# Performance work log

Measured on AMD Instinct MI355X. Metric: run time of the kernel, lower is better.

Reference implementation:

```python
import jax, jax.numpy as jnp
import numpy as np

N_NODES = 100000


def _gcn_conv(x, W, b, src, dst, n):
    # PyG GCNConv: h = x @ W; add self-loops; norm = d^-1/2[src] * d^-1/2[dst];
    # out[i] = sum_{(s->i)} norm * h[s] + b
    h = x @ W  # [N, F_out]
    deg = jax.ops.segment_sum(jnp.ones_like(dst, dtype=h.dtype), dst, num_segments=n)
    dis = jnp.where(deg > 0, jax.lax.rsqrt(jnp.maximum(deg, 1.0)), 0.0)
    norm = dis[src] * dis[dst]  # [E]
    msg = h[src] * norm[:, None]  # [E, F_out] gather + scale
    out = jax.ops.segment_sum(msg, dst, num_segments=n)  # scatter-add
    return out + b


def _add_self_loops(edge_index, n):
    loops = jnp.arange(n, dtype=edge_index.dtype)
    src = jnp.concatenate([edge_index[0], loops])
    dst = jnp.concatenate([edge_index[1], loops])
    return src, dst


def setup_inputs() -> dict:
    key = jax.random.key(0)
    k_x, k_e, k_w1, k_w2 = jax.random.split(key, 4)
    n, e, f_in, f_hid = N_NODES, 1600000, 128, 64
    x = jax.random.normal(k_x, (n, f_in), dtype=jnp.float32)
    edge_index = jax.random.randint(k_e, (2, e), 0, n, dtype=jnp.int64)
    # Glorot-ish init for weights
    W1 = jax.random.normal(k_w1, (f_in, f_hid), dtype=jnp.float32) / np.sqrt(f_in)
    b1 = jnp.zeros((f_hid,), dtype=jnp.float32)
    W2 = jax.random.normal(k_w2, (f_hid, f_hid), dtype=jnp.float32) / np.sqrt(f_hid)
    b2 = jnp.zeros((f_hid,), dtype=jnp.float32)
    return {"x": x, "edge_index": edge_index, "W1": W1, "b1": b1, "W2": W2, "b2": b2}


def reference(x, edge_index, W1, b1, W2, b2):
    n = x.shape[0]
    src, dst = _add_self_loops(edge_index, n)
    h = jax.nn.relu(_gcn_conv(x, W1, b1, src, dst, n))
    # F.dropout(training=False) in eval mode is identity
    out = _gcn_conv(h, W2, b2, src, dst, n)
    return out
```

## Files before the change

### kernel.cpp

```cpp
#include <hip/hip_runtime.h>
#include <hip/hip_bf16.h>


#define FOUT 64
#define BW 128
#define BSH 7
#define MAXB 1024
#define NCHS 512
#define CHUNK 4096
#define SLAB 3072

#define NT1 1024
#define NT2 512
#define LCOLN 2048

__device__ __forceinline__ float bf2f(unsigned int u16) {
    union { unsigned int i; float f; } c;
    c.i = u16 << 16;
    return c.f;
}
__device__ __forceinline__ unsigned short f2bf(float f) {
    union { float f; unsigned int i; } c;
    c.f = f;
    unsigned int i = c.i;
    return (unsigned short)((i + 0x7FFFu + ((i >> 16) & 1u)) >> 16);
}

typedef __attribute__((ext_vector_type(8))) short short8v;
typedef __attribute__((ext_vector_type(4))) float f32x4;

__device__ __forceinline__ void split_frag(const float* xa, short8v* Ah, short8v* Al) {
    union { unsigned int u[4]; short8v v; } H, L;
#pragma unroll
    for (int p = 0; p < 4; p++) {
        unsigned short h0 = f2bf(xa[2 * p]);
        unsigned short h1 = f2bf(xa[2 * p + 1]);
        H.u[p] = (unsigned int)h0 | ((unsigned int)h1 << 16);
        unsigned short l0 = f2bf(xa[2 * p] - bf2f(h0));
        unsigned short l1 = f2bf(xa[2 * p + 1] - bf2f(h1));
        L.u[p] = (unsigned int)l0 | ((unsigned int)l1 << 16);
    }
    *Ah = H.v;
    *Al = L.v;
}

__device__ __forceinline__ void conv_w_frag(const float* __restrict__ W,
                                            unsigned short* __restrict__ WhF,
                                            unsigned short* __restrict__ WlF,
                                            int task) {
    const int lane = task & 63;
    const int cf = (task >> 6) & 3;
    const int s = task >> 8;
    const int q = lane >> 4, m = lane & 15;
#pragma unroll
    for (int j = 0; j < 8; j++) {
        int k = s * 32 + q * 8 + j;
        float x = W[(size_t)k * 64 + cf * 16 + m];
        unsigned short h = f2bf(x);
        WhF[(size_t)task * 8 + j] = h;
        WlF[(size_t)task * 8 + j] = f2bf(x - bf2f(h));
    }
}

__global__ __launch_bounds__(512) void edge_sort(
    const int* __restrict__ src, const int* __restrict__ dst, int E,
    int* __restrict__ pk, int* __restrict__ ebuf2,
    const float* __restrict__ W1, const float* __restrict__ W2,
    unsigned short* __restrict__ whf1, unsigned short* __restrict__ wlf1,
    unsigned short* __restrict__ whf2, unsigned short* __restrict__ wlf2) {
    __shared__ int h[MAXB];
    __shared__ int lbuf[CHUNK];
    __shared__ int wt8[8];
    const int blk = blockIdx.x, t = threadIdx.x;
    const int lane = t & 63, wv = t >> 6;
    const int e0 = blk * CHUNK;
    const int chunkE = min(CHUNK, E - e0);

    int ed[CHUNK / 512], es[CHUNK / 512];
#pragma unroll
    for (int k = 0; k < CHUNK / 512; k++) {
        int e = e0 + k * 512 + t;
        bool ok = (e < E);
        ed[k] = ok ? dst[e] : -1;
        es[k] = ok ? src[e] : 0;
    }
    h[t] = 0;
    h[t + 512] = 0;
    __syncthreads();
#pragma unroll
    for (int k = 0; k < CHUNK / 512; k++)
        if (ed[k] >= 0) atomicAdd(&h[ed[k] >> BSH], 1);
    if (blk == 0) {
        for (int task = t; task < NT1 + NT2; task += 512) {
            if (task < NT1) conv_w_frag(W1, whf1, wlf1, task);
            else            conv_w_frag(W2, whf2, wlf2, task - NT1);
        }
    }
    __syncthreads();
    const int c0 = h[t], c1 = h[t + 512];

    int pv = c0;
#pragma unroll
    for (int d = 1; d < 64; d <<= 1) {
        int x = __shfl_up(pv, d);
        if (lane >= d) pv += x;
    }
    if (lane == 63) wt8[wv] = pv;
    __syncthreads();
    int woff = 0, tot0 = 0;
#pragma unroll
    for (int ww = 0; ww < 8; ww++) {
        int vw = wt8[ww];
        if (ww < wv) woff += vw;
        tot0 += vw;
    }
    const int excl0 = woff + pv - c0;
    __syncthreads();
    int pv1 = c1;
#pragma unroll
    for (int d = 1; d < 64; d <<= 1) {
        int x = __shfl_up(pv1, d);
        if (lane >= d) pv1 += x;
    }
    if (lane == 63) wt8[wv] = pv1;
    __syncthreads();
    int woff1 = 0;
#pragma unroll
    for (int ww = 0; ww < 8; ww++)
        if (ww < wv) woff1 += wt8[ww];
    const int excl1 = tot0 + woff1 + pv1 - c1;

    pk[t * NCHS + blk] = (excl0 << 16) | c0;
    pk[(t + 512) * NCHS + blk] = (excl1 << 16) | c1;

    h[t] = excl0;
    h[t + 512] = excl1;
    __syncthreads();
#pragma unroll
    for (int k = 0; k < CHUNK / 512; k++)
        if (ed[k] >= 0) {
            int b = ed[k] >> BSH;
            int r = atomicAdd(&h[b], 1);
            lbuf[r] = es[k] | ((ed[k] & (BW - 1)) << 17);
        }
    __syncthreads();
#pragma unroll
    for (int k = 0; k < CHUNK / 512; k++) {
        int i = t + k * 512;
        if (i < chunkE) ebuf2[(size_t)blk * CHUNK + i] = lbuf[i];
    }
}

__global__ __launch_bounds__(256, 3) void csr_gemm(
    const int* __restrict__ pk, const int* __restrict__ ebuf2, int nch,
    int* __restrict__ ebuf, unsigned int* __restrict__ rowinfo,
    float* __restrict__ dis, int n,
    const float* __restrict__ X, const unsigned short* __restrict__ WhF,
    const unsigned short* __restrict__ WlF, unsigned short* __restrict__ HS) {
    __shared__ int ldeg[BW];
    __shared__ float sdis[BW];
    __shared__ int wt4[4];
    __shared__ int prefL[NCHS];
    __shared__ int loffL[NCHS];
    const int b = blockIdx.x, t = threadIdx.x;
    const int node0 = b << BSH;
    const int nn = min(BW, n - node0);
    const int ebeg = b * SLAB;

    const int lane = t & 63;
    const int wvv = t >> 6;
    const int m = lane & 15;
    const int q = lane >> 4;
    const int tile0 = wvv * 2, tile1 = wvv * 2 + 1;
    const int r0 = node0 + tile0 * 16 + m;
    const int r1 = node0 + tile1 * 16 + m;
    const bool ok0 = (r0 < n), ok1 = (r1 < n);
    const float* xp0 = X + (size_t)r0 * 128 + q * 8;
    const float* xp1 = X + (size_t)r1 * 128 + q * 8;
    const float4 zf4 = make_float4(0.f, 0.f, 0.f, 0.f);

    const int pkA = (t < nch) ? pk[b * NCHS + t] : 0;
    const int pkB = (t + 256 < nch) ? pk[b * NCHS + t + 256] : 0;
#define XDECL(S) float4 xa##S##_0, xa##S##_1, xb##S##_0, xb##S##_1;
    XDECL(0) XDECL(1) XDECL(2) XDECL(3)
#undef XDECL
#define XLOAD(S)                                                             \
    if (ok0) {                                                               \
        xa##S##_0 = *(const float4*)(xp0 + (S) * 32);                        \
        xa##S##_1 = *(const float4*)(xp0 + (S) * 32 + 4);                    \
    } else { xa##S##_0 = zf4; xa##S##_1 = zf4; }                             \
    if (ok1) {                                                               \
        xb##S##_0 = *(const float4*)(xp1 + (S) * 32);                        \
        xb##S##_1 = *(const float4*)(xp1 + (S) * 32 + 4);                    \
    } else { xb##S##_0 = zf4; xb##S##_1 = zf4; }
    XLOAD(0) XLOAD(1) XLOAD(2) XLOAD(3)
#undef XLOAD

    const int cA = pkA & 0xFFFF, cB = pkB & 0xFFFF;
    int pv = cA;
#pragma unroll
    for (int d = 1; d < 64; d <<= 1) {
        int x = __shfl_up(pv, d);
        if (lane >= d) pv += x;
    }
    if (lane == 63) wt4[wvv] = pv;
    __syncthreads();
    int woff = 0, tot0 = 0;
#pragma unroll
    for (int ww = 0; ww < 4; ww++) {
        int vw = wt4[ww];
        if (ww < wvv) woff += vw;
        tot0 += vw;
    }
    const int exA = woff + pv - cA;
    __syncthreads();
    int pv1 = cB;
#pragma unroll
    for (int d = 1; d < 64; d <<= 1) {
        int x = __shfl_up(pv1, d);
        if (lane >= d) pv1 += x;
    }
    if (lane == 63) wt4[wvv] = pv1;
    __syncthreads();
    int woff1 = 0, tot1 = 0;
#pragma unroll
    for (int ww = 0; ww < 4; ww++) {
        int vw = wt4[ww];
        if (ww < wvv) woff1 += vw;
        tot1 += vw;
    }
    const int exB = tot0 + woff1 + pv1 - cB;
    const int cntE = tot0 + tot1;
    prefL[t] = exA;
    prefL[t + 256] = exB;
    loffL[t] = (int)((unsigned)pkA >> 16);
    loffL[t + 256] = (int)((unsigned)pkB >> 16);
    if (t < BW) ldeg[t] = 0;
    __syncthreads();

    int w[SLAB / 256];
#pragma unroll
    for (int k = 0; k < SLAB / 256; k++) {
        const int p = t + k * 256;
        if (p < cntE) {
            int lo = 0, hi = NCHS;
#pragma unroll
            for (int it = 0; it < 9; it++) {
                int mid = (lo + hi) >> 1;
                if (prefL[mid] <= p) lo = mid; else hi = mid;
            }
            w[k] = ebuf2[(size_t)lo * CHUNK + loffL[lo] + (p - prefL[lo])];
        } else {
            w[k] = -1;
        }
    }
#pragma unroll
    for (int k = 0; k < SLAB / 256; k++)
        if (w[k] >= 0) atomicAdd(&ldeg[w[k] >> 17], 1);
    __syncthreads();

    int v = 0, pv2 = 0;
    if (t < BW) { v = ldeg[t]; pv2 = v; }
#pragma unroll
    for (int d = 1; d < 64; d <<= 1) {
        int x = __shfl_up(pv2, d);
        if (lane >= d) pv2 += x;
    }
    if (t < BW && lane == 63) wt4[t >> 6] = pv2;
    __syncthreads();
    if (t < BW && t >= 64) pv2 += wt4[0];
    const int ex = pv2 - v;
    if (t < nn) {
        rowinfo[node0 + t] = ((unsigned int)(ebeg + ex) << 8) | (unsigned int)v;
        float dv = rsqrtf((float)v + 1.0f);
        dis[node0 + t] = dv;
        sdis[t] = dv;
    } else if (t < BW) {
        sdis[t] = 0.f;
    }
    if (t < BW) ldeg[t] = ex;
    __syncthreads();
#pragma unroll
    for (int k = 0; k < SLAB / 256; k++)
        if (w[k] >= 0) {
            int r = atomicAdd(&ldeg[w[k] >> 17], 1);
            ebuf[ebeg + r] = w[k] & 0x1FFFF;
        }

    f32x4 acc0[4], acc1[4];
#pragma unroll
    for (int cf = 0; cf < 4; cf++) { acc0[cf] = (f32x4)0.f; acc1[cf] = (f32x4)0.f; }

#define GSTEP(S)                                                                        \
    {                                                                                   \
        const unsigned short* wh = WhF + ((size_t)((S) * 4) * 64 + lane) * 8;           \
        const unsigned short* wl = WlF + ((size_t)((S) * 4) * 64 + lane) * 8;           \
        short8v Ah, Al;                                                                 \
        {                                                                               \
            const float xv[8] = {xa##S##_0.x, xa##S##_0.y, xa##S##_0.z, xa##S##_0.w,    \
                                 xa##S##_1.x, xa##S##_1.y, xa##S##_1.z, xa##S##_1.w};   \
            split_frag(xv, &Ah, &Al);                                                   \
        }                                                                               \
        _Pragma("unroll")                                                               \
        for (int cf = 0; cf < 4; cf++) {                                                \
            short8v bh = *(const short8v*)(wh + (size_t)cf * 64 * 8);                   \
            short8v bl = *(const short8v*)(wl + (size_t)cf * 64 * 8);                   \
            acc0[cf] = __builtin_amdgcn_mfma_f32_16x16x32_bf16(Ah, bh, acc0[cf], 0, 0, 0); \
            acc0[cf] = __builtin_amdgcn_mfma_f32_16x16x32_bf16(Al, bh, acc0[cf], 0, 0, 0); \
            acc0[cf] = __builtin_amdgcn_mfma_f32_16x16x32_bf16(Ah, bl, acc0[cf], 0, 0, 0); \
        }                                                                               \
        {                                                                               \
            const float xv[8] = {xb##S##_0.x, xb##S##_0.y, xb##S##_0.z, xb##S##_0.w,    \
                                 xb##S##_1.x, xb##S##_1.y, xb##S##_1.z, xb##S##_1.w};   \
            split_frag(xv, &Ah, &Al);                                                   \
        }                                                                               \
        _Pragma("unroll")                                                               \
        for (int cf = 0; cf < 4; cf++) {                                                \
            short8v bh = *(const short8v*)(wh + (size_t)cf * 64 * 8);                   \
            short8v bl = *(const short8v*)(wl + (size_t)cf * 64 * 8);                   \
            acc1[cf] = __builtin_amdgcn_mfma_f32_16x16x32_bf16(Ah, bh, acc1[cf], 0, 0, 0); \
            acc1[cf] = __builtin_amdgcn_mfma_f32_16x16x32_bf16(Al, bh, acc1[cf], 0, 0, 0); \
            acc1[cf] = __builtin_amdgcn_mfma_f32_16x16x32_bf16(Ah, bl, acc1[cf], 0, 0, 0); \
        }                                                                               \
    }
    GSTEP(0) GSTEP(1) GSTEP(2) GSTEP(3)
#undef GSTEP

#pragma unroll
    for (int r = 0; r < 4; r++) {
        int row = node0 + tile0 * 16 + q * 4 + r;
        if (row < n) {
            float dr = sdis[tile0 * 16 + q * 4 + r];
#pragma unroll
            for (int cf = 0; cf < 4; cf++)
                HS[(size_t)row * FOUT + cf * 16 + m] = f2bf(acc0[cf][r] * dr);
        }
        row = node0 + tile1 * 16 + q * 4 + r;
        if (row < n) {
            float dr = sdis[tile1 * 16 + q * 4 + r];
#pragma unroll
            for (int cf = 0; cf < 4; cf++)
                HS[(size_t)row * FOUT + cf * 16 + m] = f2bf(acc1[cf][r] * dr);
        }
    }
}

__device__ __forceinline__ void acc8(const uint4 u, float* a) {
    a[0] += bf2f(u.x & 0xFFFFu); a[1] += bf2f(u.x >> 16);
    a[2] += bf2f(u.y & 0xFFFFu); a[3] += bf2f(u.y >> 16);
    a[4] += bf2f(u.z & 0xFFFFu); a[5] += bf2f(u.z >> 16);
    a[6] += bf2f(u.w & 0xFFFFu); a[7] += bf2f(u.w >> 16);
}

__device__ __forceinline__ void gather_rows(
    const uint4* __restrict__ hsv, const int* __restrict__ lcol,
    const int* __restrict__ col, bool uselds, int off, int beg, int deg,
    int jj, float* a) {
    const int full = deg & ~3;
    if (full > 0) {
        int s0 = uselds ? lcol[off]     : col[beg];
        int s1 = uselds ? lcol[off + 1] : col[beg + 1];
        int s2 = uselds ? lcol[off + 2] : col[beg + 2];
        int s3 = uselds ? lcol[off + 3] : col[beg + 3];
        uint4 A0 = hsv[(size_t)s0 * 8 + jj];
        uint4 A1 = hsv[(size_t)s1 * 8 + jj];
        uint4 A2 = hsv[(size_t)s2 * 8 + jj];
        uint4 A3 = hsv[(size_t)s3 * 8 + jj];
        for (int p = 4; p < full; p += 4) {
            int t0 = uselds ? lcol[off + p]     : col[beg + p];
            int t1 = uselds ? lcol[off + p + 1] : col[beg + p + 1];
            int t2 = uselds ? lcol[off + p + 2] : col[beg + p + 2];
            int t3 = uselds ? lcol[off + p + 3] : col[beg + p + 3];
            uint4 B0 = hsv[(size_t)t0 * 8 + jj];
            uint4 B1 = hsv[(size_t)t1 * 8 + jj];
            uint4 B2 = hsv[(size_t)t2 * 8 + jj];
            uint4 B3 = hsv[(size_t)t3 * 8 + jj];
            acc8(A0, a); acc8(A1, a); acc8(A2, a); acc8(A3, a);
            A0 = B0; A1 = B1; A2 = B2; A3 = B3;
        }
        acc8(A0, a); acc8(A1, a); acc8(A2, a); acc8(A3, a);
    }
    for (int p = full; p < deg; p++) {
        int s = uselds ? lcol[off + p] : col[beg + p];
        acc8(hsv[(size_t)s * 8 + jj], a);
    }
}

__device__ __forceinline__ void stage_cols(
    const unsigned int* __restrict__ rowinfo, const int* __restrict__ col,
    int* lcol, int* sbs, int i0, int n, int tid) {
    if (tid == 0) {
        int last = min(i0 + 31, n - 1);
        unsigned int r0 = rowinfo[i0];
        unsigned int rl = rowinfo[last];
        int base = (int)(r0 >> 8);
        sbs[0] = base;
        sbs[1] = (int)(rl >> 8) + (int)(rl & 255u) - base;
    }
    __syncthreads();
    const int span = sbs[1];
    if (span <= LCOLN) {
        const int base = sbs[0];
        for (int k = tid; k < span; k += 256) lcol[k] = col[base + k];
    }
    __syncthreads();
}

#define OSTR 68
__global__ __launch_bounds__(256) void agg_gemm(
    const uint4* __restrict__ hsv, const unsigned int* __restrict__ rowinfo,
    const int* __restrict__ col, const float* __restrict__ dis,
    const float* __restrict__ bias,
    const unsigned short* __restrict__ WhF2, const unsigned short* __restrict__ WlF2,
    unsigned short* __restrict__ HS2, int n) {
    __shared__ float so[32 * OSTR];
    __shared__ int lcol[LCOLN];
    __shared__ int sbs[2];
    const int tid = threadIdx.x;
    const int wv = tid >> 6;
    const int lane = tid & 63;
    const int g = lane >> 3;
    const int jj = lane & 7;
    const int lrow = wv * 8 + g;
    const int i0 = blockIdx.x * 32;
    const int i = i0 + lrow;

    const unsigned int info = (i < n) ? rowinfo[i] : 0u;
    uint4 su = make_uint4(0u, 0u, 0u, 0u);
    if (i < n) su = hsv[(size_t)i * 8 + jj];

    stage_cols(rowinfo, col, lcol, sbs, i0, n, tid);
    const int base = sbs[0], span = sbs[1];
    const bool uselds = (span <= LCOLN);

    float o[8];
#pragma unroll
    for (int p = 0; p < 8; p++) o[p] = 0.f;

    if (i < n) {
        const int beg = (int)(info >> 8);
        const int deg = (int)(info & 255u);
        const int off = beg - base;

        float a[8];
        a[0] = bf2f(su.x & 0xFFFFu); a[1] = bf2f(su.x >> 16);
        a[2] = bf2f(su.y & 0xFFFFu); a[3] = bf2f(su.y >> 16);
        a[4] = bf2f(su.z & 0xFFFFu); a[5] = bf2f(su.z >> 16);
        a[6] = bf2f(su.w & 0xFFFFu); a[7] = bf2f(su.w >> 16);

        gather_rows(hsv, lcol, col, uselds, off, beg, deg, jj, a);

        float d = dis[i];
        const float4* b4 = (const float4*)bias;
        float4 bb0 = b4[jj * 2];
        float4 bb1 = b4[jj * 2 + 1];
        o[0] = fmaxf(d * a[0] + bb0.x, 0.f);
        o[1] = fmaxf(d * a[1] + bb0.y, 0.f);
        o[2] = fmaxf(d * a[2] + bb0.z, 0.f);
        o[3] = fmaxf(d * a[3] + bb0.w, 0.f);
        o[4] = fmaxf(d * a[4] + bb1.x, 0.f);
        o[5] = fmaxf(d * a[5] + bb1.y, 0.f);
        o[6] = fmaxf(d * a[6] + bb1.z, 0.f);
        o[7] = fmaxf(d * a[7] + bb1.w, 0.f);
    }
    {
        float* sp = &so[lrow * OSTR + jj * 8];
        *(float4*)sp = make_float4(o[0], o[1], o[2], o[3]);
        *(float4*)(sp + 4) = make_float4(o[4], o[5], o[6], o[7]);
    }
    __syncthreads();

    const int tile = wv >> 1;
    const int ch = wv & 1;
    const int m = lane & 15;
    const int q = lane >> 4;
    f32x4 acc[2];
    acc[0] = (f32x4)0.f;
    acc[1] = (f32x4)0.f;
#pragma unroll
    for (int s = 0; s < 2; s++) {
        const float* ap = &so[(tile * 16 + m) * OSTR + s * 32 + q * 8];
        float4 v0 = *(const float4*)ap;
        float4 v1 = *(const float4*)(ap + 4);
        const float xv[8] = {v0.x, v0.y, v0.z, v0.w, v1.x, v1.y, v1.z, v1.w};
        short8v Ah, Al;
        split_frag(xv, &Ah, &Al);
#pragma unroll
        for (int c = 0; c < 2; c++) {
            int cf = ch * 2 + c;
            const unsigned short* wh = WhF2 + ((size_t)(s * 4 + cf) * 64 + lane) * 8;
            const unsigned short* wl = WlF2 + ((size_t)(s * 4 + cf) * 64 + lane) * 8;
            short8v bh = *(const short8v*)wh;
            short8v bl = *(const short8v*)wl;
            acc[c] = __builtin_amdgcn_mfma_f32_16x16x32_bf16(Ah, bh, acc[c], 0, 0, 0);
            acc[c] = __builtin_amdgcn_mfma_f32_16x16x32_bf16(Al, bh, acc[c], 0, 0, 0);
            acc[c] = __builtin_amdgcn_mfma_f32_16x16x32_bf16(Ah, bl, acc[c], 0, 0, 0);
        }
    }
#pragma unroll
    for (int r = 0; r < 4; r++) {
        int lr = tile * 16 + q * 4 + r;
        int i2 = blockIdx.x * 32 + lr;
        if (i2 < n) {
            float dr = dis[i2];
#pragma unroll
            for (int c = 0; c < 2; c++) {
                HS2[(size_t)i2 * FOUT + (ch * 2 + c) * 16 + m] = f2bf(acc[c][r] * dr);
            }
        }
    }
}

template <bool RELU>
__global__ __launch_bounds__(256) void aggregate(
    const uint4* __restrict__ hsv, const unsigned int* __restrict__ rowinfo,
    const int* __restrict__ col, const float* __restrict__ dis,
    const float* __restrict__ bias, float* __restrict__ out, int n) {
    __shared__ int lcol[LCOLN];
    __shared__ int sbs[2];
    const int tid = threadIdx.x;
    const int wv = tid >> 6;
    const int lane = tid & 63;
    const int g = lane >> 3;
    const int jj = lane & 7;
    const int i0 = blockIdx.x * 32;
    const int i = i0 + wv * 8 + g;

    const unsigned int info = (i < n) ? rowinfo[i] : 0u;
    uint4 su = make_uint4(0u, 0u, 0u, 0u);
    if (i < n) su = hsv[(size_t)i * 8 + jj];

    stage_cols(rowinfo, col, lcol, sbs, i0, n, tid);
    const int base = sbs[0], span = sbs[1];
    const bool uselds = (span <= LCOLN);

    if (i >= n) return;

    const int beg = (int)(info >> 8);
    const int deg = (int)(info & 255u);
    const int off = beg - base;

    float a[8];
    a[0] = bf2f(su.x & 0xFFFFu); a[1] = bf2f(su.x >> 16);
    a[2] = bf2f(su.y & 0xFFFFu); a[3] = bf2f(su.y >> 16);
    a[4] = bf2f(su.z & 0xFFFFu); a[5] = bf2f(su.z >> 16);
    a[6] = bf2f(su.w & 0xFFFFu); a[7] = bf2f(su.w >> 16);

    gather_rows(hsv, lcol, col, uselds, off, beg, deg, jj, a);

    float d = dis[i];
    const float4* b4 = (const float4*)bias;
    float4 bb0 = b4[jj * 2];
    float4 bb1 = b4[jj * 2 + 1];
    float4 o0, o1;
    o0.x = d * a[0] + bb0.x; o0.y = d * a[1] + bb0.y;
    o0.z = d * a[2] + bb0.z; o0.w = d * a[3] + bb0.w;
    o1.x = d * a[4] + bb1.x; o1.y = d * a[5] + bb1.y;
    o1.z = d * a[6] + bb1.z; o1.w = d * a[7] + bb1.w;
    if (RELU) {
        o0.x = fmaxf(o0.x, 0.f); o0.y = fmaxf(o0.y, 0.f);
        o0.z = fmaxf(o0.z, 0.f); o0.w = fmaxf(o0.w, 0.f);
        o1.x = fmaxf(o1.x, 0.f); o1.y = fmaxf(o1.y, 0.f);
        o1.z = fmaxf(o1.z, 0.f); o1.w = fmaxf(o1.w, 0.f);
    }
    float4* orow = (float4*)out + (size_t)i * 16 + jj * 2;
    orow[0] = o0;
    orow[1] = o1;
}

extern "C" void kernel_launch(void* const* d_in, const int* in_sizes, int n_in,
                              void* d_out, int out_size, void* d_ws, size_t ws_size,
                              hipStream_t stream) {
    const float* x  = (const float*)d_in[0];
    const int*   ei = (const int*)d_in[1];
    const float* W1 = (const float*)d_in[2];
    const float* b1 = (const float*)d_in[3];
    const float* W2 = (const float*)d_in[4];
    const float* b2 = (const float*)d_in[5];

    const int n = in_sizes[0] / 128;
    const int E = in_sizes[1] / 2;
    const int* srcp = ei;
    const int* dstp = ei + E;

    float* out = (float*)d_out;

    const int B = (n + BW - 1) / BW;
    const int nch = (E + CHUNK - 1) / CHUNK;

    int*            pk      = (int*)d_ws;
    int*            ebuf2   = pk + (size_t)MAXB * NCHS;
    unsigned int*   rowinfo = (unsigned int*)(ebuf2 + (size_t)NCHS * CHUNK);
    float*          dis     = (float*)(rowinfo + n);
    int*            ebuf    = (int*)(dis + n);
    unsigned short* hs      = (unsigned short*)(ebuf + (size_t)B * SLAB);
    unsigned short* whf1    = hs + (size_t)n * FOUT;
    unsigned short* wlf1    = whf1 + (size_t)NT1 * 8;
    unsigned short* whf2    = wlf1 + (size_t)NT1 * 8;
    unsigned short* wlf2    = whf2 + (size_t)NT2 * 8;
    unsigned short* hs2     = wlf2 + (size_t)NT2 * 8;

    edge_sort<<<nch, 512, 0, stream>>>(srcp, dstp, E, pk, ebuf2, W1, W2,
                                       whf1, wlf1, whf2, wlf2);

    csr_gemm<<<B, 256, 0, stream>>>(pk, ebuf2, nch, ebuf, rowinfo, dis, n,
                                    x, whf1, wlf1, hs);

    agg_gemm<<<(n + 31) / 32, 256, 0, stream>>>(
        (const uint4*)hs, rowinfo, ebuf, dis, b1, whf2, wlf2, hs2, n);

    aggregate<false><<<(n + 31) / 32, 256, 0, stream>>>(
        (const uint4*)hs2, rowinfo, ebuf, dis, b2, out, n);
}
```

Measured before the change: 200.7 us.

## Halve node bucket width to 64 and give each wave one GEMM tile

Node buckets shrink from 128 to 64, so there are twice as many buckets (2048) and twice as many csr_gemm blocks, each with a smaller edge slab. The binning kernel's scan is reworked so each thread handles four consecutive buckets with a single wave-level scan. csr_gemm now gives each wave one 16-row tile instead of two, with fewer registers and higher launch bounds (6 blocks per CU), to raise occupancy and parallelism. The trade-off is a larger pk matrix and more blocks. The halved slab also leaves less headroom for buckets that receive more edges than average.

```diff
diff --git a/kernel.cpp b/kernel.cpp
--- a/kernel.cpp
+++ b/kernel.cpp
@@ -3,12 +3,12 @@
 
 
 #define FOUT 64
-#define BW 128
-#define BSH 7
-#define MAXB 1024
+#define BW 64
+#define BSH 6
+#define MAXB 2048
 #define NCHS 512
 #define CHUNK 4096
-#define SLAB 3072
+#define SLAB 1536
 
 #define NT1 1024
 #define NT2 512
@@ -84,8 +84,8 @@
         ed[k] = ok ? dst[e] : -1;
         es[k] = ok ? src[e] : 0;
     }
-    h[t] = 0;
-    h[t + 512] = 0;
+#pragma unroll
+    for (int j = 0; j < MAXB / 512; j++) h[t + 512 * j] = 0;
     __syncthreads();
 #pragma unroll
     for (int k = 0; k < CHUNK / 512; k++)
@@ -97,9 +97,12 @@
         }
     }
     __syncthreads();
-    const int c0 = h[t], c1 = h[t + 512];
-
-    int pv = c0;
+
+    int cc[4];
+#pragma unroll
+    for (int j = 0; j < 4; j++) cc[j] = h[4 * t + j];
+    const int s = cc[0] + cc[1] + cc[2] + cc[3];
+    int pv = s;
 #pragma unroll
     for (int d = 1; d < 64; d <<= 1) {
         int x = __shfl_up(pv, d);
@@ -107,34 +110,18 @@
     }
     if (lane == 63) wt8[wv] = pv;
     __syncthreads();
-    int woff = 0, tot0 = 0;
-#pragma unroll
-    for (int ww = 0; ww < 8; ww++) {
-        int vw = wt8[ww];
-        if (ww < wv) woff += vw;
-        tot0 += vw;
-    }
-    const int excl0 = woff + pv - c0;
-    __syncthreads();
-    int pv1 = c1;
-#pragma unroll
-    for (int d = 1; d < 64; d <<= 1) {
-        int x = __shfl_up(pv1, d);
-        if (lane >= d) pv1 += x;
-    }
-    if (lane == 63) wt8[wv] = pv1;
-    __syncthreads();
-    int woff1 = 0;
+    int woff = 0;
 #pragma unroll
     for (int ww = 0; ww < 8; ww++)
-        if (ww < wv) woff1 += wt8[ww];
-    const int excl1 = tot0 + woff1 + pv1 - c1;
-
-    pk[t * NCHS + blk] = (excl0 << 16) | c0;
-    pk[(t + 512) * NCHS + blk] = (excl1 << 16) | c1;
-
-    h[t] = excl0;
-    h[t + 512] = excl1;
+        if (ww < wv) woff += wt8[ww];
+    int base = woff + pv - s;
+#pragma unroll
+    for (int j = 0; j < 4; j++) {
+        const int bk = 4 * t + j;
+        pk[bk * NCHS + blk] = (base << 16) | cc[j];
+        h[bk] = base;
+        base += cc[j];
+    }
     __syncthreads();
 #pragma unroll
     for (int k = 0; k < CHUNK / 512; k++)
@@ -151,7 +138,7 @@
     }
 }
 
-__global__ __launch_bounds__(256, 3) void csr_gemm(
+__global__ __launch_bounds__(256, 6) void csr_gemm(
     const int* __restrict__ pk, const int* __restrict__ ebuf2, int nch,
     int* __restrict__ ebuf, unsigned int* __restrict__ rowinfo,
     float* __restrict__ dis, int n,
@@ -171,28 +158,22 @@
     const int wvv = t >> 6;
     const int m = lane & 15;
     const int q = lane >> 4;
-    const int tile0 = wvv * 2, tile1 = wvv * 2 + 1;
-    const int r0 = node0 + tile0 * 16 + m;
-    const int r1 = node0 + tile1 * 16 + m;
-    const bool ok0 = (r0 < n), ok1 = (r1 < n);
+    const int wrow0 = node0 + wvv * 16;
+    const int r0 = wrow0 + m;
+    const bool ok0 = (r0 < n);
     const float* xp0 = X + (size_t)r0 * 128 + q * 8;
-    const float* xp1 = X + (size_t)r1 * 128 + q * 8;
     const float4 zf4 = make_float4(0.f, 0.f, 0.f, 0.f);
 
     const int pkA = (t < nch) ? pk[b * NCHS + t] : 0;
     const int pkB = (t + 256 < nch) ? pk[b * NCHS + t + 256] : 0;
-#define XDECL(S) float4 xa##S##_0, xa##S##_1, xb##S##_0, xb##S##_1;
+#define XDECL(S) float4 xa##S##_0, xa##S##_1;
     XDECL(0) XDECL(1) XDECL(2) XDECL(3)
 #undef XDECL
 #define XLOAD(S)                                                             \
     if (ok0) {                                                               \
         xa##S##_0 = *(const float4*)(xp0 + (S) * 32);                        \
         xa##S##_1 = *(const float4*)(xp0 + (S) * 32 + 4);                    \
-    } else { xa##S##_0 = zf4; xa##S##_1 = zf4; }                             \
-    if (ok1) {                                                               \
-        xb##S##_0 = *(const float4*)(xp1 + (S) * 32);                        \
-        xb##S##_1 = *(const float4*)(xp1 + (S) * 32 + 4);                    \
-    } else { xb##S##_0 = zf4; xb##S##_1 = zf4; }
+    } else { xa##S##_0 = zf4; xa##S##_1 = zf4; }
     XLOAD(0) XLOAD(1) XLOAD(2) XLOAD(3)
 #undef XLOAD
 
@@ -266,9 +247,6 @@
         int x = __shfl_up(pv2, d);
         if (lane >= d) pv2 += x;
     }
-    if (t < BW && lane == 63) wt4[t >> 6] = pv2;
-    __syncthreads();
-    if (t < BW && t >= 64) pv2 += wt4[0];
     const int ex = pv2 - v;
     if (t < nn) {
         rowinfo[node0 + t] = ((unsigned int)(ebeg + ex) << 8) | (unsigned int)v;
@@ -287,9 +265,9 @@
             ebuf[ebeg + r] = w[k] & 0x1FFFF;
         }
 
-    f32x4 acc0[4], acc1[4];
-#pragma unroll
-    for (int cf = 0; cf < 4; cf++) { acc0[cf] = (f32x4)0.f; acc1[cf] = (f32x4)0.f; }
+    f32x4 acc0[4];
+#pragma unroll
+    for (int cf = 0; cf < 4; cf++) acc0[cf] = (f32x4)0.f;
 
 #define GSTEP(S)                                                                        \
     {                                                                                   \
@@ -309,38 +287,18 @@
             acc0[cf] = __builtin_amdgcn_mfma_f32_16x16x32_bf16(Al, bh, acc0[cf], 0, 0, 0); \
             acc0[cf] = __builtin_amdgcn_mfma_f32_16x16x32_bf16(Ah, bl, acc0[cf], 0, 0, 0); \
         }                                                                               \
-        {                                                                               \
-            const float xv[8] = {xb##S##_0.x, xb##S##_0.y, xb##S##_0.z, xb##S##_0.w,    \
-                                 xb##S##_1.x, xb##S##_1.y, xb##S##_1.z, xb##S##_1.w};   \
-            split_frag(xv, &Ah, &Al);                                                   \
-        }                                                                               \
-        _Pragma("unroll")                                                               \
-        for (int cf = 0; cf < 4; cf++) {                                                \
-            short8v bh = *(const short8v*)(wh + (size_t)cf * 64 * 8);                   \
-            short8v bl = *(const short8v*)(wl + (size_t)cf * 64 * 8);                   \
-            acc1[cf] = __builtin_amdgcn_mfma_f32_16x16x32_bf16(Ah, bh, acc1[cf], 0, 0, 0); \
-            acc1[cf] = __builtin_amdgcn_mfma_f32_16x16x32_bf16(Al, bh, acc1[cf], 0, 0, 0); \
-            acc1[cf] = __builtin_amdgcn_mfma_f32_16x16x32_bf16(Ah, bl, acc1[cf], 0, 0, 0); \
-        }                                                                               \
     }
     GSTEP(0) GSTEP(1) GSTEP(2) GSTEP(3)
 #undef GSTEP
 
 #pragma unroll
     for (int r = 0; r < 4; r++) {
-        int row = node0 + tile0 * 16 + q * 4 + r;
+        int row = wrow0 + q * 4 + r;
         if (row < n) {
-            float dr = sdis[tile0 * 16 + q * 4 + r];
+            float dr = sdis[wvv * 16 + q * 4 + r];
 #pragma unroll
             for (int cf = 0; cf < 4; cf++)
                 HS[(size_t)row * FOUT + cf * 16 + m] = f2bf(acc0[cf][r] * dr);
-        }
-        row = node0 + tile1 * 16 + q * 4 + r;
-        if (row < n) {
-            float dr = sdis[tile1 * 16 + q * 4 + r];
-#pragma unroll
-            for (int cf = 0; cf < 4; cf++)
-                HS[(size_t)row * FOUT + cf * 16 + m] = f2bf(acc1[cf][r] * dr);
         }
     }
 }
```

Measured after the change: 203.2 us. About the same (+1.3%).
